# Performance work log

Measured on AMD Instinct MI355X. Metric: run time of the kernel, lower is better.

The kernel has to match this reference:

```python
import jax, jax.numpy as jnp
import numpy as np

B, Q, K, D, H = 2, 2048, 2048, 1024, 16
HD = D // H  # 64
EPS = 1e-6  # flax LayerNorm default epsilon


def setup_inputs() -> dict:
    key = jax.random.key(0)
    ks = jax.random.split(key, 12)
    s = 1.0 / np.sqrt(D)  # lecun_normal-like scale
    inputs_q = jax.random.normal(ks[0], (B, Q, D), jnp.float32)
    bias = jax.random.normal(ks[1], (B, 1, Q, K), jnp.float32)
    mask = jax.random.randint(ks[2], (B, 1, Q, K), 0, 2).astype(jnp.bool_)
    wq = jax.random.normal(ks[3], (D, H, HD), jnp.float32) * s
    wk = jax.random.normal(ks[4], (D, H, HD), jnp.float32) * s
    wv = jax.random.normal(ks[5], (D, H, HD), jnp.float32) * s
    bq = jnp.zeros((H, HD), jnp.float32)
    bk = jnp.zeros((H, HD), jnp.float32)
    bv = jnp.zeros((H, HD), jnp.float32)
    q_scale = jnp.ones((HD,), jnp.float32)
    k_scale = jnp.ones((HD,), jnp.float32)
    wo = jax.random.normal(ks[6], (H, HD, D), jnp.float32) * s
    bo = jnp.zeros((D,), jnp.float32)
    return dict(inputs_q=inputs_q, bias=bias, mask=mask, wq=wq, bq=bq,
                wk=wk, bk=bk, wv=wv, bv=bv, q_scale=q_scale, k_scale=k_scale,
                wo=wo, bo=bo)


def _layernorm_nobias(x, scale):
    # normalize over last axis (head_dim), no bias, like flax LayerNorm(use_bias=False)
    mean = jnp.mean(x, axis=-1, keepdims=True)
    var = jnp.mean(jnp.square(x - mean), axis=-1, keepdims=True)
    return (x - mean) * jax.lax.rsqrt(var + EPS) * scale


def reference(inputs_q, bias, mask, wq, bq, wk, bk, wv, bv, q_scale, k_scale, wo, bo):
    # QKV projections (self-attention: k and v inputs default to inputs_q)
    q = jnp.einsum('bqd,dhe->bqhe', inputs_q, wq) + bq  # [B,Q,H,HD]
    k = jnp.einsum('bkd,dhe->bkhe', inputs_q, wk) + bk  # [B,K,H,HD]
    v = jnp.einsum('bkd,dhe->bkhe', inputs_q, wv) + bv  # [B,K,H,HD]
    # optional QK layernorm (normalize_qk=True)
    q = _layernorm_nobias(q, q_scale)
    k = _layernorm_nobias(k, k_scale)
    # attention weights
    q = q / jnp.sqrt(jnp.asarray(q.shape[-1], q.dtype))
    attn = jnp.einsum('bqhe,bkhe->bhqk', q, k)  # [B,H,Q,K]
    attn = attn + bias
    big_neg = jnp.finfo(q.dtype).min
    attn = jnp.where(mask, attn, big_neg)
    attn = jax.nn.softmax(attn.astype(jnp.float32), axis=-1).astype(q.dtype)
    # weighted values + output projection
    x = jnp.einsum('bhqk,bkhe->bqhe', attn, v)  # [B,Q,H,HD]
    out = jnp.einsum('bqhe,heo->bqo', x, wo) + bo  # [B,Q,D]
    return out
```

## Files before the change

kernel.cpp:

```cpp
#include <hip/hip_runtime.h>
#include <cstdint>
#include <cstddef>

typedef __bf16 bf16_t;
typedef __bf16 bf16x8 __attribute__((ext_vector_type(8)));
typedef __bf16 bf16x4 __attribute__((ext_vector_type(4)));
typedef _Float16 f16_t;
typedef _Float16 f16x4 __attribute__((ext_vector_type(4)));
typedef _Float16 f16x2 __attribute__((ext_vector_type(2)));
typedef float f32x4 __attribute__((ext_vector_type(4)));

constexpr int BB = 2, SS = 2048, DD = 1024, HH = 16, HDIM = 64;
constexpr int BS = BB * SS;
constexpr float LOG2E = 1.4426950408889634f;

__device__ __forceinline__ void glds16(const void* g, void* l) {
  __builtin_amdgcn_global_load_lds((const __attribute__((address_space(1))) void*)g,
                                   (__attribute__((address_space(3))) void*)l, 16, 0, 0);
}

__global__ __launch_bounds__(256) void prep_fused(
    const float* __restrict__ x, const float* __restrict__ wq, const float* __restrict__ wk,
    const float* __restrict__ wv, const float* __restrict__ wo, const float* __restrict__ bias,
    const int* __restrict__ mask, bf16_t* __restrict__ xb, bf16_t* __restrict__ wqkv_t,
    bf16_t* __restrict__ wo_t, f16_t* __restrict__ vmq) {
  __shared__ __align__(16) char smem[18432];
  float (*tile)[65] = (float(*)[65])smem;
  f16_t (*btile)[72] = (f16_t(*)[72])smem;
  int bid = blockIdx.x;
  int t = threadIdx.x;
  if (bid < 4096) {
    int i = bid * 256 + t;
    float4 v = ((const float4*)x)[i];
    union { bf16_t h[4]; uint2 u; } o;
    o.h[0] = (bf16_t)v.x; o.h[1] = (bf16_t)v.y; o.h[2] = (bf16_t)v.z; o.h[3] = (bf16_t)v.w;
    ((uint2*)xb)[i] = o.u;
  } else if (bid < 5120) {
    int id = bid - 4096;
    int which = id >> 8, tr = (id >> 4) & 15, tc = id & 15;
    const float* src = (which == 0) ? wq : (which == 1) ? wk : (which == 2) ? wv : wo;
    bf16_t* dst = (which < 3) ? wqkv_t : wo_t;
    int noff = (which < 3) ? which * 1024 : 0;
#pragma unroll
    for (int p = 0; p < 4; ++p) {
      int e = (p * 256 + t) * 4;
      int r = e >> 6, c = e & 63;
      float4 v = *(const float4*)&src[(size_t)(tr * 64 + r) * 1024 + tc * 64 + c];
      tile[r][c] = v.x; tile[r][c + 1] = v.y; tile[r][c + 2] = v.z; tile[r][c + 3] = v.w;
    }
    __syncthreads();
#pragma unroll
    for (int p = 0; p < 4; ++p) {
      int e = (p * 256 + t) * 4;
      int r = e >> 6, c = e & 63;
      union { bf16_t h[4]; uint2 u; } o;
#pragma unroll
      for (int j = 0; j < 4; ++j) o.h[j] = (bf16_t)tile[c + j][r];
      *(uint2*)&dst[(size_t)(noff + tc * 64 + r) * 1024 + tr * 64 + c] = o.u;
    }
  } else {
    int id = bid - 5120;
    int b = id >> 9, qt = (id >> 5) & 15, kt = id & 31;
    size_t base_in = ((size_t)(b * 2048 + qt * 128)) * 2048 + kt * 64;
#pragma unroll
    for (int p = 0; p < 4; ++p) {
      int c = p * 256 + t;
      int qr = c >> 3, k8 = (c & 7) * 8;
      const float* bp = &bias[base_in + (size_t)qr * 2048 + k8];
      const int* mp = &mask[base_in + (size_t)qr * 2048 + k8];
      float4 b0 = *(const float4*)bp;
      float4 b1 = *(const float4*)(bp + 4);
      int4 m0 = *(const int4*)mp;
      int4 m1 = *(const int4*)(mp + 4);
      union { f16_t h[8]; uint4 u; } o;
      o.h[0] = m0.x ? (f16_t)__builtin_amdgcn_exp2f(b0.x * LOG2E - 8.0f) : (f16_t)0.0f;
      o.h[1] = m0.y ? (f16_t)__builtin_amdgcn_exp2f(b0.y * LOG2E - 8.0f) : (f16_t)0.0f;
      o.h[2] = m0.z ? (f16_t)__builtin_amdgcn_exp2f(b0.z * LOG2E - 8.0f) : (f16_t)0.0f;
      o.h[3] = m0.w ? (f16_t)__builtin_amdgcn_exp2f(b0.w * LOG2E - 8.0f) : (f16_t)0.0f;
      o.h[4] = m1.x ? (f16_t)__builtin_amdgcn_exp2f(b1.x * LOG2E - 8.0f) : (f16_t)0.0f;
      o.h[5] = m1.y ? (f16_t)__builtin_amdgcn_exp2f(b1.y * LOG2E - 8.0f) : (f16_t)0.0f;
      o.h[6] = m1.z ? (f16_t)__builtin_amdgcn_exp2f(b1.z * LOG2E - 8.0f) : (f16_t)0.0f;
      o.h[7] = m1.w ? (f16_t)__builtin_amdgcn_exp2f(b1.w * LOG2E - 8.0f) : (f16_t)0.0f;
      *(uint4*)&btile[qr][k8] = o.u;
    }
    __syncthreads();
    int w = t >> 6, lane = t & 63, lo = lane & 15, quad = lane >> 4;
    size_t obase = ((size_t)(((b * 16 + qt) * 32 + kt) * 16)) * 64;
#pragma unroll
    for (int j = 0; j < 4; ++j) {
      int row = w * 32 + (j >> 1) * 16 + lo;
      int mbl = 2 * (j & 1);
      union { f16_t h[8]; uint4 u; } o;
#pragma unroll
      for (int e = 0; e < 8; ++e)
        o.h[e] = btile[row][(mbl + (e >> 2)) * 16 + quad * 4 + (e & 3)];
      ((uint4*)vmq)[obase + (w * 4 + j) * 64 + lane] = o.u;
    }
  }
}

template <bool OUT_F32, int BNT>
__global__ __launch_bounds__(256) void gemm_bt(const bf16_t* __restrict__ A,
                                               const bf16_t* __restrict__ Bt,
                                               bf16_t* __restrict__ Cb, float* __restrict__ Cf,
                                               const float* __restrict__ bias, int M, int N,
                                               int Kd) {
  constexpr int WNW = BNT / 2;
  constexpr int NFR = WNW / 16;
  __shared__ __align__(16) bf16_t As[128][32];
  __shared__ __align__(16) bf16_t Bs[BNT][32];
  int tid = threadIdx.x;
  int lane = tid & 63, w = tid >> 6;
  int lo = lane & 15, quad = lane >> 4;
  int wm = w >> 1, wn = w & 1;
  int m0 = blockIdx.y * 128, n0 = blockIdx.x * BNT;
  int srow = lane >> 2;
  int scol = (lane & 3) * 8;
  f32x4 acc[4][NFR] = {};
  for (int kk = 0; kk < Kd; kk += 32) {
#pragma unroll
    for (int t = 0; t < 2; ++t) {
      int rb = (w * 2 + t) * 16;
      glds16(&A[(size_t)(m0 + rb + srow) * Kd + kk + scol], &As[rb][0]);
      if (rb < BNT) glds16(&Bt[(size_t)(n0 + rb + srow) * Kd + kk + scol], &Bs[rb][0]);
    }
    asm volatile("s_waitcnt vmcnt(0)" ::: "memory");
    __syncthreads();
    bf16x8 am[4], bn[NFR];
#pragma unroll
    for (int i = 0; i < 4; ++i) am[i] = *(const bf16x8*)&As[wm * 64 + i * 16 + lo][quad * 8];
#pragma unroll
    for (int i = 0; i < NFR; ++i) bn[i] = *(const bf16x8*)&Bs[wn * WNW + i * 16 + lo][quad * 8];
#pragma unroll
    for (int mi = 0; mi < 4; ++mi)
#pragma unroll
      for (int ni = 0; ni < NFR; ++ni)
        acc[mi][ni] = __builtin_amdgcn_mfma_f32_16x16x32_bf16(am[mi], bn[ni], acc[mi][ni], 0, 0, 0);
    __syncthreads();
  }
#pragma unroll
  for (int mi = 0; mi < 4; ++mi) {
#pragma unroll
    for (int ni = 0; ni < NFR; ++ni) {
#pragma unroll
      for (int r = 0; r < 4; ++r) {
        int row = m0 + wm * 64 + mi * 16 + quad * 4 + r;
        int col = n0 + wn * WNW + ni * 16 + lo;
        float v = acc[mi][ni][r];
        if (OUT_F32)
          Cf[(size_t)row * N + col] = v + bias[col];
        else
          Cb[(size_t)row * N + col] = (bf16_t)v;
      }
    }
  }
}

__global__ __launch_bounds__(256) void postqkv(const bf16_t* __restrict__ Cqkv,
                                               const float* __restrict__ bq,
                                               const float* __restrict__ bk,
                                               const float* __restrict__ bv,
                                               const float* __restrict__ q_scale,
                                               const float* __restrict__ k_scale,
                                               bf16_t* __restrict__ qb, bf16_t* __restrict__ kb,
                                               f16_t* __restrict__ vt) {
  __shared__ float tile[64][65];
  int bid = blockIdx.x;
  int t = threadIdx.x;
  if (bid < 32768) {
    int mode = bid >> 14;
    int vec = (bid & 16383) * 4 + (t >> 6);
    int lane = t & 63;
    int bs = vec >> 4, h = vec & 15;
    int b = bs >> 11, s = bs & 2047;
    const float* badd = (mode == 0) ? bq : bk;
    float x = (float)Cqkv[(size_t)bs * 3072 + mode * 1024 + h * 64 + lane] + badd[h * 64 + lane];
    float sum = x;
#pragma unroll
    for (int off = 32; off >= 1; off >>= 1) sum += __shfl_xor(sum, off, 64);
    float mean = sum * (1.0f / 64.0f);
    float d = x - mean;
    float vs = d * d;
#pragma unroll
    for (int off = 32; off >= 1; off >>= 1) vs += __shfl_xor(vs, off, 64);
    float var = vs * (1.0f / 64.0f);
    const float* sc = (mode == 0) ? q_scale : k_scale;
    float y = d * rsqrtf(var + 1e-6f) * sc[lane];
    if (mode == 0) y *= 0.125f * LOG2E;
    bf16_t* dst = (mode == 0) ? qb : kb;
    int el = (mode == 0) ? lane : ((((lane >> 3) ^ (s & 7)) << 3) | (lane & 7));
    dst[(size_t)((b * 16 + h) * 2048 + s) * 64 + el] = (bf16_t)y;
  } else {
    int id2 = bid - 32768;
    int st = id2 & 31, h = (id2 >> 5) & 15, b = id2 >> 9;
#pragma unroll
    for (int p = 0; p < 2; ++p) {
      int e = (p * 256 + t) * 8;
      int r = e >> 6, c = e & 63;
      bf16x8 v8 = *(const bf16x8*)&Cqkv[(size_t)(b * SS + st * 64 + r) * 3072 + 2048 + h * 64 + c];
#pragma unroll
      for (int j = 0; j < 8; ++j) tile[r][c + j] = (float)v8[j] + bv[h * 64 + c + j];
    }
    __syncthreads();
#pragma unroll
    for (int p = 0; p < 2; ++p) {
      int e = (p * 256 + t) * 8;
      int r = e >> 6, c = e & 63;
      union { f16_t h[8]; uint4 u; } o;
#pragma unroll
      for (int j = 0; j < 8; ++j) o.h[j] = (f16_t)tile[c + j][r];
      *(uint4*)&vt[(size_t)((b * HH + h) * HDIM + r) * SS + st * 64 +
                   ((((c >> 3) ^ (r & 7)) << 3))] = o.u;
    }
  }
}

__global__ __launch_bounds__(256) void attn_kernel(const bf16_t* __restrict__ qb,
                                                   const bf16_t* __restrict__ kb,
                                                   const f16_t* __restrict__ vt,
                                                   const f16_t* __restrict__ vmq,
                                                   bf16_t* __restrict__ xout) {
  __shared__ __align__(16) bf16_t Ks[2][64][64];
  __shared__ __align__(16) f16_t Vs[2][64][64];
  int tid = threadIdx.x;
  int lane = tid & 63, w = tid >> 6;
  int lo = lane & 15, quad = lane >> 4;
  int qt = blockIdx.x, h = blockIdx.y, b = blockIdx.z;
  size_t headoff = (size_t)(b * HH + h) * SS * HDIM;
  int q0 = qt * 128 + w * 32;
  const bf16_t* kbase = kb + headoff;
  const f16_t* vbase = vt + headoff;
  const uint4* vmbase =
      (const uint4*)vmq + ((size_t)((b * 16 + qt) * 32) * 16 + w * 4) * 64 + lane;

  bf16x8 bqf[2][2];
#pragma unroll
  for (int qg = 0; qg < 2; ++qg)
#pragma unroll
    for (int ec = 0; ec < 2; ++ec)
      bqf[qg][ec] =
          *(const bf16x8*)&qb[headoff + (size_t)(q0 + qg * 16 + lo) * HDIM + ec * 32 + quad * 8];

  f16x4 ones;
#pragma unroll
  for (int j = 0; j < 4; ++j) ones[j] = (f16_t)1.0f;

  f32x4 ot[2][4] = {};
  f32x4 lacc[2] = {};

  union VM { uint4 u; f16x4 q[2]; };
  VM vr[4];

#pragma unroll
  for (int tt = 0; tt < 2; ++tt) {
    int i = w * 2 + tt;
    int r = i * 8 + (lane >> 3);
    glds16(&kbase[(size_t)r * 64 + ((lane & 7) << 3)], &Ks[0][i * 8][0]);
    glds16(&vbase[(size_t)r * SS + ((lane & 7) << 3)], &Vs[0][i * 8][0]);
  }
#pragma unroll
  for (int j = 0; j < 4; ++j) vr[j].u = vmbase[j * 64];
  asm volatile("s_waitcnt vmcnt(0)" ::: "memory");
  __syncthreads();

#pragma unroll 2
  for (int kt = 0; kt < SS / 64; ++kt) {
    int cur = kt & 1;
    VM vn[4];
    if (kt < SS / 64 - 1) {
      int k0n = (kt + 1) * 64;
#pragma unroll
      for (int tt = 0; tt < 2; ++tt) {
        int i = w * 2 + tt;
        int r = i * 8 + (lane >> 3);
        glds16(&kbase[(size_t)(k0n + r) * 64 + ((lane & 7) << 3)], &Ks[cur ^ 1][i * 8][0]);
        glds16(&vbase[(size_t)r * SS + k0n + ((lane & 7) << 3)], &Vs[cur ^ 1][i * 8][0]);
      }
#pragma unroll
      for (int j = 0; j < 4; ++j) vn[j].u = vmbase[(size_t)(kt + 1) * 1024 + j * 64];
    }

    bf16x8 ka[4][2];
#pragma unroll
    for (int mb = 0; mb < 4; ++mb) {
      const char* krow = (const char*)&Ks[cur][mb * 16 + lo][0];
#pragma unroll
      for (int ec = 0; ec < 2; ++ec)
        ka[mb][ec] = *(const bf16x8*)(krow + ((((ec << 2) | quad) ^ (lo & 7)) << 4));
    }

    f16x4 pf[2][4];
#pragma unroll
    for (int qg = 0; qg < 2; ++qg) {
#pragma unroll
      for (int mb = 0; mb < 4; ++mb) {
        f32x4 s = {};
        s = __builtin_amdgcn_mfma_f32_16x16x32_bf16(ka[mb][0], bqf[qg][0], s, 0, 0, 0);
        s = __builtin_amdgcn_mfma_f32_16x16x32_bf16(ka[mb][1], bqf[qg][1], s, 0, 0, 0);
        f16x4 p4;
        p4[0] = (f16_t)__builtin_amdgcn_exp2f(fminf(s[0], 15.0f));
        p4[1] = (f16_t)__builtin_amdgcn_exp2f(fminf(s[1], 15.0f));
        p4[2] = (f16_t)__builtin_amdgcn_exp2f(fminf(s[2], 15.0f));
        p4[3] = (f16_t)__builtin_amdgcn_exp2f(fminf(s[3], 15.0f));
        pf[qg][mb] = p4 * vr[qg * 2 + (mb >> 1)].q[mb & 1];
      }
    }

#pragma unroll
    for (int mb = 0; mb < 4; ++mb) {
#pragma unroll
      for (int eb = 0; eb < 4; ++eb) {
        const char* vrow = (const char*)&Vs[cur][eb * 16 + lo][0];
        f16x4 va = *(const f16x4*)(vrow + (((((mb << 1) | (quad >> 1)) ^ (lo & 7)) << 4) |
                                           ((quad & 1) << 3)));
#pragma unroll
        for (int qg = 0; qg < 2; ++qg)
          ot[qg][eb] = __builtin_amdgcn_mfma_f32_16x16x16f16(va, pf[qg][mb], ot[qg][eb], 0, 0, 0);
      }
#pragma unroll
      for (int qg = 0; qg < 2; ++qg)
        lacc[qg] = __builtin_amdgcn_mfma_f32_16x16x16f16(ones, pf[qg][mb], lacc[qg], 0, 0, 0);
    }

    asm volatile("s_waitcnt vmcnt(0)" ::: "memory");
    __syncthreads();
    if (kt < SS / 64 - 1) {
#pragma unroll
      for (int j = 0; j < 4; ++j) vr[j] = vn[j];
    }
  }

#pragma unroll
  for (int qg = 0; qg < 2; ++qg) {
    float rl = 1.0f / lacc[qg][0];
    int q = q0 + qg * 16 + lo;
#pragma unroll
    for (int eb = 0; eb < 4; ++eb) {
      union { bf16_t h4[4]; uint2 u; } o;
#pragma unroll
      for (int r = 0; r < 4; ++r) o.h4[r] = (bf16_t)(ot[qg][eb][r] * rl);
      *(uint2*)&xout[(size_t)(b * SS + q) * DD + h * 64 + eb * 16 + quad * 4] = o.u;
    }
  }
}

extern "C" void kernel_launch(void* const* d_in, const int* in_sizes, int n_in, void* d_out,
                              int out_size, void* d_ws, size_t ws_size, hipStream_t stream) {
  const float* inputs_q = (const float*)d_in[0];
  const float* bias = (const float*)d_in[1];
  const int* mask = (const int*)d_in[2];
  const float* wq = (const float*)d_in[3];
  const float* bq = (const float*)d_in[4];
  const float* wk = (const float*)d_in[5];
  const float* bk = (const float*)d_in[6];
  const float* wv = (const float*)d_in[7];
  const float* bv = (const float*)d_in[8];
  const float* q_scale = (const float*)d_in[9];
  const float* k_scale = (const float*)d_in[10];
  const float* wo = (const float*)d_in[11];
  const float* bo = (const float*)d_in[12];
  float* out = (float*)d_out;

  char* ws = (char*)d_ws;
  bf16_t* wo_t   = (bf16_t*)(ws);
  f16_t*  vmq    = (f16_t*)(ws + ((size_t)2 << 20));
  bf16_t* cqkv   = (bf16_t*)(ws + ((size_t)19 << 20));
  bf16_t* xattn  = (bf16_t*)(ws + ((size_t)19 << 20));
  bf16_t* xb     = (bf16_t*)(ws + ((size_t)43 << 20));
  bf16_t* qb2    = (bf16_t*)(ws + ((size_t)43 << 20));
  bf16_t* wqkv_t = (bf16_t*)(ws + ((size_t)51 << 20));
  bf16_t* kb2    = (bf16_t*)(ws + ((size_t)51 << 20));
  f16_t*  vtb    = (f16_t*)(ws + ((size_t)59 << 20));

  prep_fused<<<6144, 256, 0, stream>>>(inputs_q, wq, wk, wv, wo, bias, mask, xb, wqkv_t, wo_t, vmq);
  gemm_bt<false, 128><<<dim3(24, 32), 256, 0, stream>>>(xb, wqkv_t, cqkv, nullptr, nullptr, BS,
                                                        3072, DD);
  postqkv<<<33792, 256, 0, stream>>>(cqkv, bq, bk, bv, q_scale, k_scale, qb2, kb2, vtb);
  attn_kernel<<<dim3(SS / 128, HH, BB), 256, 0, stream>>>(qb2, kb2, vtb, vmq, xattn);
  gemm_bt<true, 64><<<dim3(16, 32), 256, 0, stream>>>(xattn, wo_t, nullptr, out, bo, BS, 1024, DD);
}
```

Measured before the change: 303.7 us.

## Triple-buffer attention with 64-query tiles, batch postqkv rows, widen output GEMM tile

The attention kernel now processes 64 queries per block (16 per wave) instead of 128, doubling the grid. It uses a three-stage LDS ring with a partial vmcnt wait and s_setprio around the MFMA section, so loads run two tiles ahead. The mask/bias tile layout written by prep is reordered to match the new tiling. The postqkv layernorm path now handles 8 vectors per wave, shrinking the grid from 33792 to 5120 blocks. The output GEMM switches to a 128-wide N tile. Smaller query tiles halve K/V reuse per block, and the deeper pipeline raises LDS use to 48KB per block.

```diff
diff --git a/kernel.cpp b/kernel.cpp
--- a/kernel.cpp
+++ b/kernel.cpp
@@ -7,7 +7,6 @@
 typedef __bf16 bf16x4 __attribute__((ext_vector_type(4)));
 typedef _Float16 f16_t;
 typedef _Float16 f16x4 __attribute__((ext_vector_type(4)));
-typedef _Float16 f16x2 __attribute__((ext_vector_type(2)));
 typedef float f32x4 __attribute__((ext_vector_type(4)));
 
 constexpr int BB = 2, SS = 2048, DD = 1024, HH = 16, HDIM = 64;
@@ -84,17 +83,19 @@
       *(uint4*)&btile[qr][k8] = o.u;
     }
     __syncthreads();
-    int w = t >> 6, lane = t & 63, lo = lane & 15, quad = lane >> 4;
-    size_t obase = ((size_t)(((b * 16 + qt) * 32 + kt) * 16)) * 64;
+    int w_p = t >> 6, lane = t & 63, lo = lane & 15, quad = lane >> 4;
+    int qt2l = w_p >> 1;
 #pragma unroll
     for (int j = 0; j < 4; ++j) {
-      int row = w * 32 + (j >> 1) * 16 + lo;
-      int mbl = 2 * (j & 1);
+      int wa = (w_p & 1) * 2 + (j >> 1);
+      int jj = j & 1;
+      int row = qt2l * 64 + wa * 16 + lo;
       union { f16_t h[8]; uint4 u; } o;
 #pragma unroll
       for (int e = 0; e < 8; ++e)
-        o.h[e] = btile[row][(mbl + (e >> 2)) * 16 + quad * 4 + (e & 3)];
-      ((uint4*)vmq)[obase + (w * 4 + j) * 64 + lane] = o.u;
+        o.h[e] = btile[row][(jj * 2 + (e >> 2)) * 16 + quad * 4 + (e & 3)];
+      size_t chunk = ((size_t)((b * 32 + qt * 2 + qt2l) * 32 + kt) * 8) + wa * 2 + jj;
+      ((uint4*)vmq)[chunk * 64 + lane] = o.u;
     }
   }
 }
@@ -167,31 +168,35 @@
   __shared__ float tile[64][65];
   int bid = blockIdx.x;
   int t = threadIdx.x;
-  if (bid < 32768) {
-    int mode = bid >> 14;
-    int vec = (bid & 16383) * 4 + (t >> 6);
+  if (bid < 4096) {
+    int mode = bid >> 11;
     int lane = t & 63;
-    int bs = vec >> 4, h = vec & 15;
-    int b = bs >> 11, s = bs & 2047;
     const float* badd = (mode == 0) ? bq : bk;
-    float x = (float)Cqkv[(size_t)bs * 3072 + mode * 1024 + h * 64 + lane] + badd[h * 64 + lane];
-    float sum = x;
-#pragma unroll
-    for (int off = 32; off >= 1; off >>= 1) sum += __shfl_xor(sum, off, 64);
-    float mean = sum * (1.0f / 64.0f);
-    float d = x - mean;
-    float vs = d * d;
-#pragma unroll
-    for (int off = 32; off >= 1; off >>= 1) vs += __shfl_xor(vs, off, 64);
-    float var = vs * (1.0f / 64.0f);
     const float* sc = (mode == 0) ? q_scale : k_scale;
-    float y = d * rsqrtf(var + 1e-6f) * sc[lane];
-    if (mode == 0) y *= 0.125f * LOG2E;
     bf16_t* dst = (mode == 0) ? qb : kb;
-    int el = (mode == 0) ? lane : ((((lane >> 3) ^ (s & 7)) << 3) | (lane & 7));
-    dst[(size_t)((b * 16 + h) * 2048 + s) * 64 + el] = (bf16_t)y;
+    int vb = (bid & 2047) * 32 + (t >> 6) * 8;
+#pragma unroll
+    for (int i = 0; i < 8; ++i) {
+      int vec = vb + i;
+      int bs = vec >> 4, h = vec & 15;
+      int b = bs >> 11, s = bs & 2047;
+      float x = (float)Cqkv[(size_t)bs * 3072 + mode * 1024 + h * 64 + lane] + badd[h * 64 + lane];
+      float sum = x;
+#pragma unroll
+      for (int off = 32; off >= 1; off >>= 1) sum += __shfl_xor(sum, off, 64);
+      float mean = sum * (1.0f / 64.0f);
+      float d = x - mean;
+      float vs = d * d;
+#pragma unroll
+      for (int off = 32; off >= 1; off >>= 1) vs += __shfl_xor(vs, off, 64);
+      float var = vs * (1.0f / 64.0f);
+      float y = d * rsqrtf(var + 1e-6f) * sc[lane];
+      if (mode == 0) y *= 0.125f * LOG2E;
+      int el = (mode == 0) ? lane : ((((lane >> 3) ^ (s & 7)) << 3) | (lane & 7));
+      dst[(size_t)((b * 16 + h) * 2048 + s) * 64 + el] = (bf16_t)y;
+    }
   } else {
-    int id2 = bid - 32768;
+    int id2 = bid - 4096;
     int st = id2 & 31, h = (id2 >> 5) & 15, b = id2 >> 9;
 #pragma unroll
     for (int p = 0; p < 2; ++p) {
@@ -215,132 +220,120 @@
   }
 }
 
-__global__ __launch_bounds__(256) void attn_kernel(const bf16_t* __restrict__ qb,
-                                                   const bf16_t* __restrict__ kb,
-                                                   const f16_t* __restrict__ vt,
-                                                   const f16_t* __restrict__ vmq,
-                                                   bf16_t* __restrict__ xout) {
-  __shared__ __align__(16) bf16_t Ks[2][64][64];
-  __shared__ __align__(16) f16_t Vs[2][64][64];
+__global__ __launch_bounds__(256, 3) void attn_kernel(const bf16_t* __restrict__ qb,
+                                                      const bf16_t* __restrict__ kb,
+                                                      const f16_t* __restrict__ vt,
+                                                      const f16_t* __restrict__ vmq,
+                                                      bf16_t* __restrict__ xout) {
+  __shared__ __align__(16) char lds[3][16384];
   int tid = threadIdx.x;
   int lane = tid & 63, w = tid >> 6;
   int lo = lane & 15, quad = lane >> 4;
-  int qt = blockIdx.x, h = blockIdx.y, b = blockIdx.z;
+  int qt2 = blockIdx.x, h = blockIdx.y, b = blockIdx.z;
   size_t headoff = (size_t)(b * HH + h) * SS * HDIM;
-  int q0 = qt * 128 + w * 32;
+  int q0 = qt2 * 64 + w * 16;
   const bf16_t* kbase = kb + headoff;
   const f16_t* vbase = vt + headoff;
-  const uint4* vmbase =
-      (const uint4*)vmq + ((size_t)((b * 16 + qt) * 32) * 16 + w * 4) * 64 + lane;
-
-  bf16x8 bqf[2][2];
-#pragma unroll
-  for (int qg = 0; qg < 2; ++qg)
-#pragma unroll
-    for (int ec = 0; ec < 2; ++ec)
-      bqf[qg][ec] =
-          *(const bf16x8*)&qb[headoff + (size_t)(q0 + qg * 16 + lo) * HDIM + ec * 32 + quad * 8];
+  const uint4* vmtile =
+      (const uint4*)vmq + ((size_t)((b * 32 + qt2) * 32) * 8 + w * 2) * 64 + lane;
+
+  bf16x8 bqf[2];
+#pragma unroll
+  for (int ec = 0; ec < 2; ++ec)
+    bqf[ec] = *(const bf16x8*)&qb[headoff + (size_t)(q0 + lo) * HDIM + ec * 32 + quad * 8];
 
   f16x4 ones;
 #pragma unroll
   for (int j = 0; j < 4; ++j) ones[j] = (f16_t)1.0f;
 
-  f32x4 ot[2][4] = {};
-  f32x4 lacc[2] = {};
-
-  union VM { uint4 u; f16x4 q[2]; };
-  VM vr[4];
-
-#pragma unroll
-  for (int tt = 0; tt < 2; ++tt) {
-    int i = w * 2 + tt;
-    int r = i * 8 + (lane >> 3);
-    glds16(&kbase[(size_t)r * 64 + ((lane & 7) << 3)], &Ks[0][i * 8][0]);
-    glds16(&vbase[(size_t)r * SS + ((lane & 7) << 3)], &Vs[0][i * 8][0]);
-  }
-#pragma unroll
-  for (int j = 0; j < 4; ++j) vr[j].u = vmbase[j * 64];
-  asm volatile("s_waitcnt vmcnt(0)" ::: "memory");
-  __syncthreads();
-
-#pragma unroll 2
+  f32x4 ot[4] = {};
+  f32x4 lacc = {};
+
+  union VM { uint4 u[2]; f16x4 q[4]; };
+  VM vr, vn, tm;
+
+  char* bcur = lds[0];
+  char* bnxt = lds[1];
+  char* bfar = lds[2];
+
+  auto stage = [&](int kt, char* dst) {
+    int k0 = kt * 64;
+#pragma unroll
+    for (int tt = 0; tt < 2; ++tt) {
+      int i = w * 2 + tt;
+      int r = i * 8 + (lane >> 3);
+      glds16(&kbase[(size_t)(k0 + r) * 64 + ((lane & 7) << 3)], dst + i * 1024);
+      glds16(&vbase[(size_t)r * SS + k0 + ((lane & 7) << 3)], dst + 8192 + i * 1024);
+    }
+  };
+
+  stage(0, bcur);
+  vr.u[0] = vmtile[0]; vr.u[1] = vmtile[64];
+  stage(1, bnxt);
+  vn.u[0] = vmtile[512]; vn.u[1] = vmtile[512 + 64];
+
+#pragma unroll 1
   for (int kt = 0; kt < SS / 64; ++kt) {
-    int cur = kt & 1;
-    VM vn[4];
-    if (kt < SS / 64 - 1) {
-      int k0n = (kt + 1) * 64;
-#pragma unroll
-      for (int tt = 0; tt < 2; ++tt) {
-        int i = w * 2 + tt;
-        int r = i * 8 + (lane >> 3);
-        glds16(&kbase[(size_t)(k0n + r) * 64 + ((lane & 7) << 3)], &Ks[cur ^ 1][i * 8][0]);
-        glds16(&vbase[(size_t)r * SS + k0n + ((lane & 7) << 3)], &Vs[cur ^ 1][i * 8][0]);
+    if (kt == SS / 64 - 1)
+      asm volatile("s_waitcnt vmcnt(0)" ::: "memory");
+    else
+      asm volatile("s_waitcnt vmcnt(6)" ::: "memory");
+    __builtin_amdgcn_s_barrier();
+    if (kt + 2 < SS / 64) {
+      size_t o = (size_t)(kt + 2) * 512;
+      tm.u[0] = vmtile[o]; tm.u[1] = vmtile[o + 64];
+      stage(kt + 2, bfar);
+    }
+
+    __builtin_amdgcn_s_setprio(1);
+    bf16x8 ka[4][2];
+#pragma unroll
+    for (int mb = 0; mb < 4; ++mb)
+#pragma unroll
+      for (int ec = 0; ec < 2; ++ec)
+        ka[mb][ec] = *(const bf16x8*)(bcur + (mb * 16 + lo) * 128 +
+                                      ((((ec << 2) | quad) ^ (lo & 7)) << 4));
+
+    f16x4 pf[4];
+#pragma unroll
+    for (int mb = 0; mb < 4; ++mb) {
+      f32x4 s = {};
+      s = __builtin_amdgcn_mfma_f32_16x16x32_bf16(ka[mb][0], bqf[0], s, 0, 0, 0);
+      s = __builtin_amdgcn_mfma_f32_16x16x32_bf16(ka[mb][1], bqf[1], s, 0, 0, 0);
+      f16x4 p4;
+      p4[0] = (f16_t)__builtin_amdgcn_exp2f(fminf(s[0], 15.0f));
+      p4[1] = (f16_t)__builtin_amdgcn_exp2f(fminf(s[1], 15.0f));
+      p4[2] = (f16_t)__builtin_amdgcn_exp2f(fminf(s[2], 15.0f));
+      p4[3] = (f16_t)__builtin_amdgcn_exp2f(fminf(s[3], 15.0f));
+      pf[mb] = p4 * vr.q[mb];
+    }
+
+#pragma unroll
+    for (int mb = 0; mb < 4; ++mb) {
+#pragma unroll
+      for (int eb = 0; eb < 4; ++eb) {
+        f16x4 va = *(const f16x4*)(bcur + 8192 + (eb * 16 + lo) * 128 +
+                                   (((((mb << 1) | (quad >> 1)) ^ (lo & 7)) << 4) |
+                                    ((quad & 1) << 3)));
+        ot[eb] = __builtin_amdgcn_mfma_f32_16x16x16f16(va, pf[mb], ot[eb], 0, 0, 0);
       }
-#pragma unroll
-      for (int j = 0; j < 4; ++j) vn[j].u = vmbase[(size_t)(kt + 1) * 1024 + j * 64];
-    }
-
-    bf16x8 ka[4][2];
-#pragma unroll
-    for (int mb = 0; mb < 4; ++mb) {
-      const char* krow = (const char*)&Ks[cur][mb * 16 + lo][0];
-#pragma unroll
-      for (int ec = 0; ec < 2; ++ec)
-        ka[mb][ec] = *(const bf16x8*)(krow + ((((ec << 2) | quad) ^ (lo & 7)) << 4));
-    }
-
-    f16x4 pf[2][4];
-#pragma unroll
-    for (int qg = 0; qg < 2; ++qg) {
-#pragma unroll
-      for (int mb = 0; mb < 4; ++mb) {
-        f32x4 s = {};
-        s = __builtin_amdgcn_mfma_f32_16x16x32_bf16(ka[mb][0], bqf[qg][0], s, 0, 0, 0);
-        s = __builtin_amdgcn_mfma_f32_16x16x32_bf16(ka[mb][1], bqf[qg][1], s, 0, 0, 0);
-        f16x4 p4;
-        p4[0] = (f16_t)__builtin_amdgcn_exp2f(fminf(s[0], 15.0f));
-        p4[1] = (f16_t)__builtin_amdgcn_exp2f(fminf(s[1], 15.0f));
-        p4[2] = (f16_t)__builtin_amdgcn_exp2f(fminf(s[2], 15.0f));
-        p4[3] = (f16_t)__builtin_amdgcn_exp2f(fminf(s[3], 15.0f));
-        pf[qg][mb] = p4 * vr[qg * 2 + (mb >> 1)].q[mb & 1];
-      }
-    }
-
-#pragma unroll
-    for (int mb = 0; mb < 4; ++mb) {
-#pragma unroll
-      for (int eb = 0; eb < 4; ++eb) {
-        const char* vrow = (const char*)&Vs[cur][eb * 16 + lo][0];
-        f16x4 va = *(const f16x4*)(vrow + (((((mb << 1) | (quad >> 1)) ^ (lo & 7)) << 4) |
-                                           ((quad & 1) << 3)));
-#pragma unroll
-        for (int qg = 0; qg < 2; ++qg)
-          ot[qg][eb] = __builtin_amdgcn_mfma_f32_16x16x16f16(va, pf[qg][mb], ot[qg][eb], 0, 0, 0);
-      }
-#pragma unroll
-      for (int qg = 0; qg < 2; ++qg)
-        lacc[qg] = __builtin_amdgcn_mfma_f32_16x16x16f16(ones, pf[qg][mb], lacc[qg], 0, 0, 0);
-    }
-
-    asm volatile("s_waitcnt vmcnt(0)" ::: "memory");
-    __syncthreads();
-    if (kt < SS / 64 - 1) {
-#pragma unroll
-      for (int j = 0; j < 4; ++j) vr[j] = vn[j];
-    }
-  }
-
-#pragma unroll
-  for (int qg = 0; qg < 2; ++qg) {
-    float rl = 1.0f / lacc[qg][0];
-    int q = q0 + qg * 16 + lo;
-#pragma unroll
-    for (int eb = 0; eb < 4; ++eb) {
-      union { bf16_t h4[4]; uint2 u; } o;
-#pragma unroll
-      for (int r = 0; r < 4; ++r) o.h4[r] = (bf16_t)(ot[qg][eb][r] * rl);
-      *(uint2*)&xout[(size_t)(b * SS + q) * DD + h * 64 + eb * 16 + quad * 4] = o.u;
-    }
+      lacc = __builtin_amdgcn_mfma_f32_16x16x16f16(ones, pf[mb], lacc, 0, 0, 0);
+    }
+    __builtin_amdgcn_s_setprio(0);
+
+    vr = vn;
+    if (kt + 2 < SS / 64) vn = tm;
+    char* t0 = bcur; bcur = bnxt; bnxt = bfar; bfar = t0;
+  }
+
+  float rl = 1.0f / lacc[0];
+  int q = q0 + lo;
+#pragma unroll
+  for (int eb = 0; eb < 4; ++eb) {
+    union { bf16_t h4[4]; uint2 u; } o;
+#pragma unroll
+    for (int r = 0; r < 4; ++r) o.h4[r] = (bf16_t)(ot[eb][r] * rl);
+    *(uint2*)&xout[(size_t)(b * SS + q) * DD + h * 64 + eb * 16 + quad * 4] = o.u;
   }
 }
 
@@ -375,7 +368,7 @@
   prep_fused<<<6144, 256, 0, stream>>>(inputs_q, wq, wk, wv, wo, bias, mask, xb, wqkv_t, wo_t, vmq);
   gemm_bt<false, 128><<<dim3(24, 32), 256, 0, stream>>>(xb, wqkv_t, cqkv, nullptr, nullptr, BS,
                                                         3072, DD);
-  postqkv<<<33792, 256, 0, stream>>>(cqkv, bq, bk, bv, q_scale, k_scale, qb2, kb2, vtb);
-  attn_kernel<<<dim3(SS / 128, HH, BB), 256, 0, stream>>>(qb2, kb2, vtb, vmq, xattn);
-  gemm_bt<true, 64><<<dim3(16, 32), 256, 0, stream>>>(xattn, wo_t, nullptr, out, bo, BS, 1024, DD);
-}
+  postqkv<<<5120, 256, 0, stream>>>(cqkv, bq, bk, bv, q_scale, k_scale, qb2, kb2, vtb);
+  attn_kernel<<<dim3(SS / 64, HH, BB), 256, 0, stream>>>(qb2, kb2, vtb, vmq, xattn);
+  gemm_bt<true, 128><<<dim3(8, 32), 256, 0, stream>>>(xattn, wo_t, nullptr, out, bo, BS, 1024, DD);
+}
```

Measured after the change: 307.9 us. Within noise of the previous version (+1.4%).

## Triple-buffer attention loads, remap GEMM blocks per XCD, batch postqkv rows per wave

Applied to the files above, without the earlier changes.

The attention kernel now uses four LDS stages with a prefetch distance of two tiles. It waits with vmcnt(8) instead of draining all loads each iteration, sets s_setprio around the MFMA sections, and uses launch_bounds(256,2). The GEMM remaps block ids so consecutive ids go to the same XCD group, which should improve L2 locality. postqkv processes 8 vectors per wave with far fewer blocks, cutting launch overhead. The extra LDS stages (64KB) and register pressure may reduce occupancy.

```diff
diff --git a/kernel.cpp b/kernel.cpp
--- a/kernel.cpp
+++ b/kernel.cpp
@@ -7,7 +7,6 @@
 typedef __bf16 bf16x4 __attribute__((ext_vector_type(4)));
 typedef _Float16 f16_t;
 typedef _Float16 f16x4 __attribute__((ext_vector_type(4)));
-typedef _Float16 f16x2 __attribute__((ext_vector_type(2)));
 typedef float f32x4 __attribute__((ext_vector_type(4)));
 
 constexpr int BB = 2, SS = 2048, DD = 1024, HH = 16, HDIM = 64;
@@ -113,7 +112,11 @@
   int lane = tid & 63, w = tid >> 6;
   int lo = lane & 15, quad = lane >> 4;
   int wm = w >> 1, wn = w & 1;
-  int m0 = blockIdx.y * 128, n0 = blockIdx.x * BNT;
+  int nbx = gridDim.x;
+  int nwg = nbx * gridDim.y;
+  int lid = blockIdx.y * nbx + blockIdx.x;
+  int sid = (lid & 7) * (nwg >> 3) + (lid >> 3);
+  int m0 = (sid / nbx) * 128, n0 = (sid % nbx) * BNT;
   int srow = lane >> 2;
   int scol = (lane & 3) * 8;
   f32x4 acc[4][NFR] = {};
@@ -167,31 +170,35 @@
   __shared__ float tile[64][65];
   int bid = blockIdx.x;
   int t = threadIdx.x;
-  if (bid < 32768) {
-    int mode = bid >> 14;
-    int vec = (bid & 16383) * 4 + (t >> 6);
+  if (bid < 4096) {
+    int mode = bid >> 11;
     int lane = t & 63;
-    int bs = vec >> 4, h = vec & 15;
-    int b = bs >> 11, s = bs & 2047;
     const float* badd = (mode == 0) ? bq : bk;
-    float x = (float)Cqkv[(size_t)bs * 3072 + mode * 1024 + h * 64 + lane] + badd[h * 64 + lane];
-    float sum = x;
-#pragma unroll
-    for (int off = 32; off >= 1; off >>= 1) sum += __shfl_xor(sum, off, 64);
-    float mean = sum * (1.0f / 64.0f);
-    float d = x - mean;
-    float vs = d * d;
-#pragma unroll
-    for (int off = 32; off >= 1; off >>= 1) vs += __shfl_xor(vs, off, 64);
-    float var = vs * (1.0f / 64.0f);
     const float* sc = (mode == 0) ? q_scale : k_scale;
-    float y = d * rsqrtf(var + 1e-6f) * sc[lane];
-    if (mode == 0) y *= 0.125f * LOG2E;
     bf16_t* dst = (mode == 0) ? qb : kb;
-    int el = (mode == 0) ? lane : ((((lane >> 3) ^ (s & 7)) << 3) | (lane & 7));
-    dst[(size_t)((b * 16 + h) * 2048 + s) * 64 + el] = (bf16_t)y;
+    int vb = (bid & 2047) * 32 + (t >> 6) * 8;
+#pragma unroll
+    for (int i = 0; i < 8; ++i) {
+      int vec = vb + i;
+      int bs = vec >> 4, h = vec & 15;
+      int b = bs >> 11, s = bs & 2047;
+      float x = (float)Cqkv[(size_t)bs * 3072 + mode * 1024 + h * 64 + lane] + badd[h * 64 + lane];
+      float sum = x;
+#pragma unroll
+      for (int off = 32; off >= 1; off >>= 1) sum += __shfl_xor(sum, off, 64);
+      float mean = sum * (1.0f / 64.0f);
+      float d = x - mean;
+      float vs = d * d;
+#pragma unroll
+      for (int off = 32; off >= 1; off >>= 1) vs += __shfl_xor(vs, off, 64);
+      float var = vs * (1.0f / 64.0f);
+      float y = d * rsqrtf(var + 1e-6f) * sc[lane];
+      if (mode == 0) y *= 0.125f * LOG2E;
+      int el = (mode == 0) ? lane : ((((lane >> 3) ^ (s & 7)) << 3) | (lane & 7));
+      dst[(size_t)((b * 16 + h) * 2048 + s) * 64 + el] = (bf16_t)y;
+    }
   } else {
-    int id2 = bid - 32768;
+    int id2 = bid - 4096;
     int st = id2 & 31, h = (id2 >> 5) & 15, b = id2 >> 9;
 #pragma unroll
     for (int p = 0; p < 2; ++p) {
@@ -215,13 +222,66 @@
   }
 }
 
-__global__ __launch_bounds__(256) void attn_kernel(const bf16_t* __restrict__ qb,
-                                                   const bf16_t* __restrict__ kb,
-                                                   const f16_t* __restrict__ vt,
-                                                   const f16_t* __restrict__ vmq,
-                                                   bf16_t* __restrict__ xout) {
-  __shared__ __align__(16) bf16_t Ks[2][64][64];
-  __shared__ __align__(16) f16_t Vs[2][64][64];
+#define ATTN_TILE(KT, CUR, STG, VMC)                                                          \
+  {                                                                                           \
+    if ((KT) == 31) { asm volatile("s_waitcnt vmcnt(0)" ::: "memory"); }                      \
+    else            { asm volatile("s_waitcnt vmcnt(8)" ::: "memory"); }                      \
+    __builtin_amdgcn_s_barrier();                                                             \
+    if ((KT) + 2 < 32) {                                                                      \
+      int k0n = ((KT) + 2) * 64;                                                              \
+      _Pragma("unroll") for (int tt = 0; tt < 2; ++tt) {                                      \
+        int i = w * 2 + tt;                                                                   \
+        int r = i * 8 + (lane >> 3);                                                          \
+        glds16(&kbase[(size_t)(k0n + r) * 64 + ((lane & 7) << 3)], (STG) + i * 1024);         \
+        glds16(&vbase[(size_t)r * SS + k0n + ((lane & 7) << 3)], (STG) + 8192 + i * 1024);    \
+      }                                                                                       \
+    }                                                                                         \
+    __builtin_amdgcn_s_setprio(1);                                                            \
+    bf16x8 ka[4][2];                                                                          \
+    _Pragma("unroll") for (int mb = 0; mb < 4; ++mb)                                          \
+      _Pragma("unroll") for (int ec = 0; ec < 2; ++ec)                                        \
+        ka[mb][ec] = *(const bf16x8*)((CUR) + (mb * 16 + lo) * 128 +                          \
+                                      ((((ec << 2) | quad) ^ (lo & 7)) << 4));                \
+    f16x4 pf[2][4];                                                                           \
+    _Pragma("unroll") for (int qg = 0; qg < 2; ++qg)                                          \
+      _Pragma("unroll") for (int mb = 0; mb < 4; ++mb) {                                      \
+        f32x4 s = {};                                                                         \
+        s = __builtin_amdgcn_mfma_f32_16x16x32_bf16(ka[mb][0], bqf[qg][0], s, 0, 0, 0);       \
+        s = __builtin_amdgcn_mfma_f32_16x16x32_bf16(ka[mb][1], bqf[qg][1], s, 0, 0, 0);       \
+        f16x4 p4;                                                                             \
+        p4[0] = (f16_t)__builtin_amdgcn_exp2f(fminf(s[0], 15.0f));                            \
+        p4[1] = (f16_t)__builtin_amdgcn_exp2f(fminf(s[1], 15.0f));                            \
+        p4[2] = (f16_t)__builtin_amdgcn_exp2f(fminf(s[2], 15.0f));                            \
+        p4[3] = (f16_t)__builtin_amdgcn_exp2f(fminf(s[3], 15.0f));                            \
+        pf[qg][mb] = p4 * VMC[qg * 2 + (mb >> 1)].q[mb & 1];                                  \
+      }                                                                                       \
+    __builtin_amdgcn_s_setprio(0);                                                            \
+    if ((KT) + 2 < 32) {           \
+      _Pragma("unroll") for (int j = 0; j < 4; ++j)                                           \
+        VMC[j].u = vmtile[(size_t)((KT) + 2) * 1024 + j * 64];                                \
+    }                                                                                         \
+    __builtin_amdgcn_s_setprio(1);                                                            \
+    _Pragma("unroll") for (int mb = 0; mb < 4; ++mb) {                                        \
+      _Pragma("unroll") for (int eb = 0; eb < 4; ++eb) {                                      \
+        f16x4 va = *(const f16x4*)((CUR) + 8192 + (eb * 16 + lo) * 128 +                      \
+                                   (((((mb << 1) | (quad >> 1)) ^ (lo & 7)) << 4) |           \
+                                    ((quad & 1) << 3)));                                      \
+        _Pragma("unroll") for (int qg = 0; qg < 2; ++qg)                                      \
+          ot[qg][eb] =                                                                        \
+              __builtin_amdgcn_mfma_f32_16x16x16f16(va, pf[qg][mb], ot[qg][eb], 0, 0, 0);     \
+      }                                                                                       \
+      _Pragma("unroll") for (int qg = 0; qg < 2; ++qg)                                        \
+        lacc[qg] = __builtin_amdgcn_mfma_f32_16x16x16f16(ones, pf[qg][mb], lacc[qg], 0, 0, 0);\
+    }                                                                                         \
+    __builtin_amdgcn_s_setprio(0);                                                            \
+  }
+
+__global__ __launch_bounds__(256, 2) void attn_kernel(const bf16_t* __restrict__ qb,
+                                                      const bf16_t* __restrict__ kb,
+                                                      const f16_t* __restrict__ vt,
+                                                      const f16_t* __restrict__ vmq,
+                                                      bf16_t* __restrict__ xout) {
+  __shared__ __align__(16) char lds[4][16384];
   int tid = threadIdx.x;
   int lane = tid & 63, w = tid >> 6;
   int lo = lane & 15, quad = lane >> 4;
@@ -230,7 +290,7 @@
   int q0 = qt * 128 + w * 32;
   const bf16_t* kbase = kb + headoff;
   const f16_t* vbase = vt + headoff;
-  const uint4* vmbase =
+  const uint4* vmtile =
       (const uint4*)vmq + ((size_t)((b * 16 + qt) * 32) * 16 + w * 4) * 64 + lane;
 
   bf16x8 bqf[2][2];
@@ -249,85 +309,33 @@
   f32x4 lacc[2] = {};
 
   union VM { uint4 u; f16x4 q[2]; };
-  VM vr[4];
+  VM vma[4], vmb[4];
 
 #pragma unroll
   for (int tt = 0; tt < 2; ++tt) {
     int i = w * 2 + tt;
     int r = i * 8 + (lane >> 3);
-    glds16(&kbase[(size_t)r * 64 + ((lane & 7) << 3)], &Ks[0][i * 8][0]);
-    glds16(&vbase[(size_t)r * SS + ((lane & 7) << 3)], &Vs[0][i * 8][0]);
-  }
-#pragma unroll
-  for (int j = 0; j < 4; ++j) vr[j].u = vmbase[j * 64];
-  asm volatile("s_waitcnt vmcnt(0)" ::: "memory");
-  __syncthreads();
-
-#pragma unroll 2
-  for (int kt = 0; kt < SS / 64; ++kt) {
-    int cur = kt & 1;
-    VM vn[4];
-    if (kt < SS / 64 - 1) {
-      int k0n = (kt + 1) * 64;
-#pragma unroll
-      for (int tt = 0; tt < 2; ++tt) {
-        int i = w * 2 + tt;
-        int r = i * 8 + (lane >> 3);
-        glds16(&kbase[(size_t)(k0n + r) * 64 + ((lane & 7) << 3)], &Ks[cur ^ 1][i * 8][0]);
-        glds16(&vbase[(size_t)r * SS + k0n + ((lane & 7) << 3)], &Vs[cur ^ 1][i * 8][0]);
-      }
-#pragma unroll
-      for (int j = 0; j < 4; ++j) vn[j].u = vmbase[(size_t)(kt + 1) * 1024 + j * 64];
-    }
-
-    bf16x8 ka[4][2];
-#pragma unroll
-    for (int mb = 0; mb < 4; ++mb) {
-      const char* krow = (const char*)&Ks[cur][mb * 16 + lo][0];
-#pragma unroll
-      for (int ec = 0; ec < 2; ++ec)
-        ka[mb][ec] = *(const bf16x8*)(krow + ((((ec << 2) | quad) ^ (lo & 7)) << 4));
-    }
-
-    f16x4 pf[2][4];
-#pragma unroll
-    for (int qg = 0; qg < 2; ++qg) {
-#pragma unroll
-      for (int mb = 0; mb < 4; ++mb) {
-        f32x4 s = {};
-        s = __builtin_amdgcn_mfma_f32_16x16x32_bf16(ka[mb][0], bqf[qg][0], s, 0, 0, 0);
-        s = __builtin_amdgcn_mfma_f32_16x16x32_bf16(ka[mb][1], bqf[qg][1], s, 0, 0, 0);
-        f16x4 p4;
-        p4[0] = (f16_t)__builtin_amdgcn_exp2f(fminf(s[0], 15.0f));
-        p4[1] = (f16_t)__builtin_amdgcn_exp2f(fminf(s[1], 15.0f));
-        p4[2] = (f16_t)__builtin_amdgcn_exp2f(fminf(s[2], 15.0f));
-        p4[3] = (f16_t)__builtin_amdgcn_exp2f(fminf(s[3], 15.0f));
-        pf[qg][mb] = p4 * vr[qg * 2 + (mb >> 1)].q[mb & 1];
-      }
-    }
-
-#pragma unroll
-    for (int mb = 0; mb < 4; ++mb) {
-#pragma unroll
-      for (int eb = 0; eb < 4; ++eb) {
-        const char* vrow = (const char*)&Vs[cur][eb * 16 + lo][0];
-        f16x4 va = *(const f16x4*)(vrow + (((((mb << 1) | (quad >> 1)) ^ (lo & 7)) << 4) |
-                                           ((quad & 1) << 3)));
-#pragma unroll
-        for (int qg = 0; qg < 2; ++qg)
-          ot[qg][eb] = __builtin_amdgcn_mfma_f32_16x16x16f16(va, pf[qg][mb], ot[qg][eb], 0, 0, 0);
-      }
-#pragma unroll
-      for (int qg = 0; qg < 2; ++qg)
-        lacc[qg] = __builtin_amdgcn_mfma_f32_16x16x16f16(ones, pf[qg][mb], lacc[qg], 0, 0, 0);
-    }
-
-    asm volatile("s_waitcnt vmcnt(0)" ::: "memory");
-    __syncthreads();
-    if (kt < SS / 64 - 1) {
-#pragma unroll
-      for (int j = 0; j < 4; ++j) vr[j] = vn[j];
-    }
+    glds16(&kbase[(size_t)r * 64 + ((lane & 7) << 3)], lds[0] + i * 1024);
+    glds16(&vbase[(size_t)r * SS + ((lane & 7) << 3)], lds[0] + 8192 + i * 1024);
+  }
+#pragma unroll
+  for (int j = 0; j < 4; ++j) vma[j].u = vmtile[j * 64];
+#pragma unroll
+  for (int tt = 0; tt < 2; ++tt) {
+    int i = w * 2 + tt;
+    int r = i * 8 + (lane >> 3);
+    glds16(&kbase[(size_t)(64 + r) * 64 + ((lane & 7) << 3)], lds[1] + i * 1024);
+    glds16(&vbase[(size_t)r * SS + 64 + ((lane & 7) << 3)], lds[1] + 8192 + i * 1024);
+  }
+#pragma unroll
+  for (int j = 0; j < 4; ++j) vmb[j].u = vmtile[1024 + j * 64];
+
+#pragma unroll 1
+  for (int kt0 = 0; kt0 < 32; kt0 += 4) {
+    ATTN_TILE(kt0 + 0, lds[0], lds[2], vma)
+    ATTN_TILE(kt0 + 1, lds[1], lds[3], vmb)
+    ATTN_TILE(kt0 + 2, lds[2], lds[0], vma)
+    ATTN_TILE(kt0 + 3, lds[3], lds[1], vmb)
   }
 
 #pragma unroll
@@ -375,7 +383,7 @@
   prep_fused<<<6144, 256, 0, stream>>>(inputs_q, wq, wk, wv, wo, bias, mask, xb, wqkv_t, wo_t, vmq);
   gemm_bt<false, 128><<<dim3(24, 32), 256, 0, stream>>>(xb, wqkv_t, cqkv, nullptr, nullptr, BS,
                                                         3072, DD);
-  postqkv<<<33792, 256, 0, stream>>>(cqkv, bq, bk, bv, q_scale, k_scale, qb2, kb2, vtb);
+  postqkv<<<5120, 256, 0, stream>>>(cqkv, bq, bk, bv, q_scale, k_scale, qb2, kb2, vtb);
   attn_kernel<<<dim3(SS / 128, HH, BB), 256, 0, stream>>>(qb2, kb2, vtb, vmq, xattn);
   gemm_bt<true, 64><<<dim3(16, 32), 256, 0, stream>>>(xattn, wo_t, nullptr, out, bo, BS, 1024, DD);
 }
```

New measurement: 285.8 us. -5.9%, faster.
